# Performance work log

Measured on AMD Instinct MI355X. Metric: run time of the kernel, lower is better.

The kernel has to match this reference:

```python
import jax, jax.numpy as jnp
import numpy as np

EPS = 1e-6


def setup_inputs() -> dict:
    key = jax.random.key(0)
    kH, kE1, kE2, kM, kW = jax.random.split(key, 5)
    B, N, D, E, L = 16, 2048, 64, 32768, 2
    H = jax.random.normal(kH, (B, N, D), dtype=jnp.float32)
    src = jax.random.randint(kE1, (B, 1, E), 0, N)
    dst = jax.random.randint(kE2, (B, 1, E), 0, N)
    edge_index = jnp.concatenate([src, dst], axis=1)  # [B, 2, E]
    m = jax.random.uniform(kM, (B, E), dtype=jnp.float32)
    W = jax.random.normal(kW, (L, D, D), dtype=jnp.float32) * (1.0 / np.sqrt(D))
    return {"H": H, "edge_index": edge_index, "m": m, "W": W}


def reference(H, edge_index, m, W):
    # H: [B, N, D]; edge_index: [B, 2, E] int; m: [B, E]; W: [L, D, D]
    B, N, _ = H.shape
    L = W.shape[0]
    bidx = jnp.arange(B)[:, None]          # [B, 1] broadcasts against [B, E]
    src = edge_index[:, 0, :]
    dst = edge_index[:, 1, :]
    A = jnp.zeros((B, N, N), dtype=H.dtype)
    # batched scatter: A[b, src, dst] = m; A[b, dst, src] = m (symmetric fill)
    A = A.at[bidx, src, dst].set(m)
    A = A.at[bidx, dst, src].set(m)
    A = A + jnp.eye(N, dtype=H.dtype)[None]  # add self loops
    deg = jnp.clip(A.sum(axis=-1), EPS)       # [B, N]
    dis = deg ** -0.5
    A_norm = dis[:, :, None] * A * dis[:, None, :]  # D^-1/2 A D^-1/2
    X = H
    for l in range(L):
        X = jnp.einsum('bnm,bmd->bnd', A_norm, X)
        X = jnp.einsum('bnd,ed->bne', X, W[l])  # Linear: X @ W^T
        if l < L - 1:
            X = jax.nn.gelu(X, approximate=False)  # torch GELU (exact erf); dropout in eval mode
    return X
```

## Files before the change

### kernel.cpp

```cpp
#include <hip/hip_runtime.h>
#include <stdint.h>
#include <math.h>

#define BATCH 16
#define NNODE 2048
#define DDIM  64
#define NEDGE 32768
#define SEG   32
#define SLOTS 128
#define NROWS (BATCH*NNODE)
#define RPB   64

__global__ void k_build(const int* __restrict__ ei, const float* __restrict__ m,
                        uint32_t* __restrict__ cnt4, uint2* __restrict__ entries) {
    __shared__ uint32_t cntS[RPB];
    __shared__ uint32_t keyS[RPB][SEG];
    __shared__ float    valS[RPB][SEG];

    int b  = blockIdx.x & 15;
    int gh = blockIdx.x >> 4;
    int r0 = (gh >> 2) * RPB;
    int q  = gh & 3;
    int t  = threadIdx.x;

    if (t < RPB) cntS[t] = 0u;
    __syncthreads();

    const int*   eb = ei + (size_t)b * 2 * NEDGE;
    const float* mb = m  + (size_t)b * NEDGE;
    int e0 = q * (NEDGE / 4);

    for (int i = 0; i < 8; ++i) {
        int e4 = e0 + i * 1024 + t * 4;
        int4   s4 = *(const int4*)(eb + e4);
        int4   d4 = *(const int4*)(eb + NEDGE + e4);
        float4 m4 = *(const float4*)(mb + e4);
        #pragma unroll
        for (int j = 0; j < 4; ++j) {
            int   src = j == 0 ? s4.x : j == 1 ? s4.y : j == 2 ? s4.z : s4.w;
            int   dst = j == 0 ? d4.x : j == 1 ? d4.y : j == 2 ? d4.z : d4.w;
            float mv  = j == 0 ? m4.x : j == 1 ? m4.y : j == 2 ? m4.z : m4.w;
            int e  = e4 + j;
            int rs = src - r0;
            if ((unsigned)rs < RPB) {
                uint32_t p = atomicAdd(&cntS[rs], 1u);
                if (p < SEG) { keyS[rs][p] = (uint32_t)dst | ((uint32_t)e << 11); valS[rs][p] = mv; }
            }
            int rd = dst - r0;
            if ((unsigned)rd < RPB) {
                uint32_t p = atomicAdd(&cntS[rd], 1u);
                if (p < SEG) { keyS[rd][p] = (uint32_t)src | ((uint32_t)(NEDGE + e) << 11); valS[rd][p] = mv; }
            }
        }
    }
    __syncthreads();

    int lane = t & 63;
    int wid  = t >> 6;
    int pos  = lane & 31;
    int sub  = lane >> 5;
    for (int rr = 0; rr < 8; ++rr) {
        int r  = wid * 16 + rr * 2 + sub;
        int rg = b * NNODE + r0 + r;
        int k  = (int)min(cntS[r], (uint32_t)SEG);
        size_t base = (size_t)rg * SLOTS + q * SEG;
        if (pos < k)
            entries[base + pos] = make_uint2(keyS[r][pos], __float_as_uint(valS[r][pos]));
        if (pos == 0) cnt4[rg * 4 + q] = (uint32_t)k;
    }
}

__global__ void k_dedupe(const uint32_t* __restrict__ cnt4, uint2* __restrict__ entries,
                         uint32_t* __restrict__ cnt_fin,
                         float* __restrict__ dis, float* __restrict__ self) {
    int b    = blockIdx.x & 15;
    int w    = b * NNODE + (blockIdx.x >> 4) * 4 + (threadIdx.x >> 6);
    int lane = threadIdx.x & 63;
    uint4 kq = ((const uint4*)cnt4)[w];
    int k0 = (int)kq.x, k1 = (int)kq.y, k2 = (int)kq.z, k3 = (int)kq.w;
    size_t base = (size_t)w * SLOTS;
    int pos = lane & 31;
    int klo = (lane < 32) ? k0 : k1;
    int khi = (lane < 32) ? k2 : k3;

    uint32_t key0 = 0u, key1 = 0u;
    float v0 = 0.f, v1 = 0.f;
    bool a0 = pos < klo;
    bool a1 = pos < khi;
    if (a0) { uint2 kv = entries[base + lane];      key0 = kv.x; v0 = __uint_as_float(kv.y); }
    if (a1) { uint2 kv = entries[base + 64 + lane]; key1 = kv.x; v1 = __uint_as_float(kv.y); }
    uint32_t c0 = key0 & 2047u, p0 = key0 >> 11;
    uint32_t c1 = key1 & 2047u, p1 = key1 >> 11;

    #define KILL(ks) { uint32_t cs = (ks) & 2047u, ps = (ks) >> 11; \
        a0 = a0 && !((c0 == cs) && (p0 < ps)); \
        a1 = a1 && !((c1 == cs) && (p1 < ps)); }
    for (int s = 0; s < k0; ++s) KILL(__builtin_amdgcn_readlane(key0, s))
    for (int s = 0; s < k1; ++s) KILL(__builtin_amdgcn_readlane(key0, 32 + s))
    for (int s = 0; s < k2; ++s) KILL(__builtin_amdgcn_readlane(key1, s))
    for (int s = 0; s < k3; ++s) KILL(__builtin_amdgcn_readlane(key1, 32 + s))
    #undef KILL

    float sum = (a0 ? v0 : 0.f) + (a1 ? v1 : 0.f);
    for (int off = 32; off; off >>= 1) sum += __shfl_xor(sum, off, 64);
    float deg = fmaxf(1.0f + sum, 1e-6f);
    if (lane == 0) {
        float di = 1.0f / sqrtf(deg);
        dis[w]  = di;
        self[w] = di * di;
    }

    unsigned long long m0 = __ballot(a0);
    unsigned long long m1 = __ballot(a1);
    unsigned long long below = (1ull << lane) - 1ull;
    int n0 = __popcll(m0);
    if (a0) entries[base + __popcll(m0 & below)]      = make_uint2(key0, __float_as_uint(v0));
    if (a1) entries[base + n0 + __popcll(m1 & below)] = make_uint2(key1, __float_as_uint(v1));
    if (lane == 0) cnt_fin[w] = (uint32_t)(n0 + __popcll(m1));
}

__global__ void k_layer(const float* __restrict__ Xin, const float* __restrict__ W,
                        float* __restrict__ Xout,
                        const uint32_t* __restrict__ cnt_fin, const uint2* __restrict__ entries,
                        const float* __restrict__ dis, const float* __restrict__ self,
                        int dogelu) {
    __shared__ float WT[64 * 65];
    int Lb = blockIdx.x;
    int b  = Lb & 15;
    int rb = Lb >> 4;
    int t  = threadIdx.x;

    #pragma unroll
    for (int i = 0; i < 16; ++i) {
        int idx = i * 256 + t;
        WT[(idx & 63) * 65 + (idx >> 6)] = W[idx];
    }
    __syncthreads();

    int lane = t & 63;
    int wid  = t >> 6;
    const float* Xb   = Xin + (size_t)b * NNODE * DDIM;
    const char*  Xc   = (const char*)Xb + lane * 4;
    const float* disB = dis + (b << 11);

    float accv[2];
    #pragma unroll
    for (int rr = 0; rr < 2; ++rr) {
        int row = rb * 8 + wid * 2 + rr;
        int rg  = b * NNODE + row;
        int k   = (int)cnt_fin[rg];
        size_t base = (size_t)rg * SLOTS;

        uint32_t kA = 0u, vA = 0u, kB = 0u, vB = 0u;
        if (lane < k)      { uint2 kv = entries[base + lane];      kA = kv.x; vA = kv.y; }
        if (lane + 64 < k) { uint2 kv = entries[base + 64 + lane]; kB = kv.x; vB = kv.y; }

        float dr = disB[row];
        int   colA = (int)(kA & 2047u);
        uint32_t offA = (uint32_t)colA << 8;
        uint32_t wAu  = __float_as_uint(__uint_as_float(vA) * dr * disB[colA]);
        int   colB = (int)(kB & 2047u);
        uint32_t offB = (uint32_t)colB << 8;
        uint32_t wBu  = __float_as_uint(__uint_as_float(vB) * dr * disB[colB]);

        float acc0 = self[rg] * Xb[(size_t)row * DDIM + lane];
        float acc1 = 0.f, acc2 = 0.f, acc3 = 0.f;

        int k0 = k < 64 ? k : 64;
        int e = 0;
        for (; e + 16 <= k0; e += 16) {
            float xv0, xv1, xv2, xv3, xv4, xv5, xv6, xv7;
            float xv8, xv9, xva, xvb, xvc, xvd, xve, xvf;
            float w0, w1, w2, w3, w4, w5, w6, w7;
            float w8, w9, wa, wb, wc, wd, we, wf;
            #define G(idx, X, Wv) { \
                uint32_t o = __builtin_amdgcn_readlane(offA, e + idx); \
                Wv = __uint_as_float(__builtin_amdgcn_readlane(wAu, e + idx)); \
                X = *(const float*)(Xc + o); }
            G(0, xv0, w0)  G(1, xv1, w1)  G(2, xv2, w2)  G(3, xv3, w3)
            G(4, xv4, w4)  G(5, xv5, w5)  G(6, xv6, w6)  G(7, xv7, w7)
            G(8, xv8, w8)  G(9, xv9, w9)  G(10, xva, wa) G(11, xvb, wb)
            G(12, xvc, wc) G(13, xvd, wd) G(14, xve, we) G(15, xvf, wf)
            #undef G
            acc0 = fmaf(w0, xv0, acc0); acc1 = fmaf(w1, xv1, acc1);
            acc2 = fmaf(w2, xv2, acc2); acc3 = fmaf(w3, xv3, acc3);
            acc0 = fmaf(w4, xv4, acc0); acc1 = fmaf(w5, xv5, acc1);
            acc2 = fmaf(w6, xv6, acc2); acc3 = fmaf(w7, xv7, acc3);
            acc0 = fmaf(w8, xv8, acc0); acc1 = fmaf(w9, xv9, acc1);
            acc2 = fmaf(wa, xva, acc2); acc3 = fmaf(wb, xvb, acc3);
            acc0 = fmaf(wc, xvc, acc0); acc1 = fmaf(wd, xvd, acc1);
            acc2 = fmaf(we, xve, acc2); acc3 = fmaf(wf, xvf, acc3);
        }
        for (; e + 4 <= k0; e += 4) {
            uint32_t o0 = __builtin_amdgcn_readlane(offA, e);
            uint32_t o1 = __builtin_amdgcn_readlane(offA, e + 1);
            uint32_t o2 = __builtin_amdgcn_readlane(offA, e + 2);
            uint32_t o3 = __builtin_amdgcn_readlane(offA, e + 3);
            float w0 = __uint_as_float(__builtin_amdgcn_readlane(wAu, e));
            float w1 = __uint_as_float(__builtin_amdgcn_readlane(wAu, e + 1));
            float w2 = __uint_as_float(__builtin_amdgcn_readlane(wAu, e + 2));
            float w3 = __uint_as_float(__builtin_amdgcn_readlane(wAu, e + 3));
            acc0 = fmaf(w0, *(const float*)(Xc + o0), acc0);
            acc1 = fmaf(w1, *(const float*)(Xc + o1), acc1);
            acc2 = fmaf(w2, *(const float*)(Xc + o2), acc2);
            acc3 = fmaf(w3, *(const float*)(Xc + o3), acc3);
        }
        for (; e < k0; ++e) {
            uint32_t o = __builtin_amdgcn_readlane(offA, e);
            float wv = __uint_as_float(__builtin_amdgcn_readlane(wAu, e));
            acc0 = fmaf(wv, *(const float*)(Xc + o), acc0);
        }
        for (e = 64; e < k; ++e) {
            uint32_t o = __builtin_amdgcn_readlane(offB, e - 64);
            float wv = __uint_as_float(__builtin_amdgcn_readlane(wBu, e - 64));
            acc1 = fmaf(wv, *(const float*)(Xc + o), acc1);
        }
        accv[rr] = (acc0 + acc1) + (acc2 + acc3);
    }

    float sa = accv[0], sb = accv[1];
    float ya = 0.f, yb = 0.f;
    #pragma unroll
    for (int d = 0; d < 64; ++d) {
        float wt = WT[d * 65 + lane];
        ya = fmaf(__uint_as_float(__builtin_amdgcn_readlane(__float_as_uint(sa), d)), wt, ya);
        yb = fmaf(__uint_as_float(__builtin_amdgcn_readlane(__float_as_uint(sb), d)), wt, yb);
    }
    if (dogelu) {
        ya = 0.5f * ya * (1.0f + erff(ya * 0.70710678118654752440f));
        yb = 0.5f * yb * (1.0f + erff(yb * 0.70710678118654752440f));
    }
    int row0 = rb * 8 + wid * 2;
    Xout[((size_t)b * NNODE + row0)     * DDIM + lane] = ya;
    Xout[((size_t)b * NNODE + row0 + 1) * DDIM + lane] = yb;
}

extern "C" void kernel_launch(void* const* d_in, const int* in_sizes, int n_in,
                              void* d_out, int out_size, void* d_ws, size_t ws_size,
                              hipStream_t stream) {
    const float* H  = (const float*)d_in[0];
    const int*   ei = (const int*)d_in[1];
    const float* m  = (const float*)d_in[2];
    const float* W  = (const float*)d_in[3];
    float* out = (float*)d_out;

    char* ws = (char*)d_ws;
    uint32_t* cnt4    = (uint32_t*)ws;
    uint32_t* cnt_fin = (uint32_t*)(ws + (512 << 10));
    float*    dis     = (float*)(ws + (640 << 10));
    float*    self    = (float*)(ws + (768 << 10));
    uint2*    entries = (uint2*)(ws + (896 << 10));
    float*    X2      = (float*)(ws + (896 << 10) + (size_t)NROWS * SLOTS * 8);

    k_build <<<BATCH * (NNODE / RPB) * 4, 256, 0, stream>>>(ei, m, cnt4, entries);
    k_dedupe<<<NROWS / 4, 256, 0, stream>>>(cnt4, entries, cnt_fin, dis, self);
    k_layer <<<4096, 256, 0, stream>>>(H,  W,        X2,  cnt_fin, entries, dis, self, 1);
    k_layer <<<4096, 256, 0, stream>>>(X2, W + 4096, out, cnt_fin, entries, dis, self, 0);
}
```

Baseline: 173.8 us.

## Fuse all phases into one cooperative persistent kernel with grid syncs

Merges the build, dedupe and two layer kernels into a single cooperative kernel of 1024 blocks that separates the phases with grid.sync(), removing three launch gaps. Each block now handles more rows (RPB 128 and 32 rows per block per layer), and SEG drops from 32 to 30 so the shared scratch fits more blocks per CU. If cooperative launch is unavailable it falls back to four separate kernels. The trade-offs are grid-barrier cost, lower parallelism per phase, and a smaller per-quarter slot cap, which drops more entries when a row overflows.

Measured after the change: 279.5 us. 1.61x slower.

```diff
diff --git a/kernel.cpp b/kernel.cpp
--- a/kernel.cpp
+++ b/kernel.cpp
@@ -1,27 +1,31 @@
 #include <hip/hip_runtime.h>
+#include <hip/hip_cooperative_groups.h>
 #include <stdint.h>
 #include <math.h>
+
+namespace cg = cooperative_groups;
 
 #define BATCH 16
 #define NNODE 2048
 #define DDIM  64
 #define NEDGE 32768
-#define SEG   32
-#define SLOTS 128
+#define SEG   30
+#define SLOTS (4*SEG)
 #define NROWS (BATCH*NNODE)
-#define RPB   64
-
-__global__ void k_build(const int* __restrict__ ei, const float* __restrict__ m,
-                        uint32_t* __restrict__ cnt4, uint2* __restrict__ entries) {
-    __shared__ uint32_t cntS[RPB];
-    __shared__ uint32_t keyS[RPB][SEG];
-    __shared__ float    valS[RPB][SEG];
-
-    int b  = blockIdx.x & 15;
-    int gh = blockIdx.x >> 4;
+#define RPB   128
+#define SMEMW (128 + 2*128*SEG)
+
+__device__ __forceinline__ void phase_build(
+        int idx, int t, const int* __restrict__ ei, const float* __restrict__ m,
+        uint32_t* __restrict__ cnt4, uint2* __restrict__ entries, uint32_t* smem) {
+    uint32_t* cntS = smem;
+    uint32_t* keyS = smem + 128;
+    float*    valS = (float*)(smem + 128 + 128 * SEG);
+
+    int b  = idx & 15;
+    int gh = idx >> 4;
     int r0 = (gh >> 2) * RPB;
     int q  = gh & 3;
-    int t  = threadIdx.x;
 
     if (t < RPB) cntS[t] = 0u;
     __syncthreads();
@@ -44,195 +48,236 @@
             int rs = src - r0;
             if ((unsigned)rs < RPB) {
                 uint32_t p = atomicAdd(&cntS[rs], 1u);
-                if (p < SEG) { keyS[rs][p] = (uint32_t)dst | ((uint32_t)e << 11); valS[rs][p] = mv; }
+                if (p < SEG) { keyS[rs * SEG + p] = (uint32_t)dst | ((uint32_t)e << 11); valS[rs * SEG + p] = mv; }
             }
             int rd = dst - r0;
             if ((unsigned)rd < RPB) {
                 uint32_t p = atomicAdd(&cntS[rd], 1u);
-                if (p < SEG) { keyS[rd][p] = (uint32_t)src | ((uint32_t)(NEDGE + e) << 11); valS[rd][p] = mv; }
-            }
-        }
-    }
-    __syncthreads();
-
-    int lane = t & 63;
-    int wid  = t >> 6;
-    int pos  = lane & 31;
-    int sub  = lane >> 5;
-    for (int rr = 0; rr < 8; ++rr) {
-        int r  = wid * 16 + rr * 2 + sub;
+                if (p < SEG) { keyS[rd * SEG + p] = (uint32_t)src | ((uint32_t)(NEDGE + e) << 11); valS[rd * SEG + p] = mv; }
+            }
+        }
+    }
+    __syncthreads();
+
+    int lane = t & 63, wid = t >> 6;
+    int pos = lane & 31, sub = lane >> 5;
+    for (int rr = 0; rr < 16; ++rr) {
+        int r  = wid * 32 + rr * 2 + sub;
         int rg = b * NNODE + r0 + r;
         int k  = (int)min(cntS[r], (uint32_t)SEG);
         size_t base = (size_t)rg * SLOTS + q * SEG;
         if (pos < k)
-            entries[base + pos] = make_uint2(keyS[r][pos], __float_as_uint(valS[r][pos]));
+            entries[base + pos] = make_uint2(keyS[r * SEG + pos], __float_as_uint(valS[r * SEG + pos]));
         if (pos == 0) cnt4[rg * 4 + q] = (uint32_t)k;
     }
 }
 
-__global__ void k_dedupe(const uint32_t* __restrict__ cnt4, uint2* __restrict__ entries,
-                         uint32_t* __restrict__ cnt_fin,
-                         float* __restrict__ dis, float* __restrict__ self) {
-    int b    = blockIdx.x & 15;
-    int w    = b * NNODE + (blockIdx.x >> 4) * 4 + (threadIdx.x >> 6);
-    int lane = threadIdx.x & 63;
-    uint4 kq = ((const uint4*)cnt4)[w];
-    int k0 = (int)kq.x, k1 = (int)kq.y, k2 = (int)kq.z, k3 = (int)kq.w;
-    size_t base = (size_t)w * SLOTS;
-    int pos = lane & 31;
-    int klo = (lane < 32) ? k0 : k1;
-    int khi = (lane < 32) ? k2 : k3;
-
-    uint32_t key0 = 0u, key1 = 0u;
-    float v0 = 0.f, v1 = 0.f;
-    bool a0 = pos < klo;
-    bool a1 = pos < khi;
-    if (a0) { uint2 kv = entries[base + lane];      key0 = kv.x; v0 = __uint_as_float(kv.y); }
-    if (a1) { uint2 kv = entries[base + 64 + lane]; key1 = kv.x; v1 = __uint_as_float(kv.y); }
-    uint32_t c0 = key0 & 2047u, p0 = key0 >> 11;
-    uint32_t c1 = key1 & 2047u, p1 = key1 >> 11;
-
-    #define KILL(ks) { uint32_t cs = (ks) & 2047u, ps = (ks) >> 11; \
-        a0 = a0 && !((c0 == cs) && (p0 < ps)); \
-        a1 = a1 && !((c1 == cs) && (p1 < ps)); }
-    for (int s = 0; s < k0; ++s) KILL(__builtin_amdgcn_readlane(key0, s))
-    for (int s = 0; s < k1; ++s) KILL(__builtin_amdgcn_readlane(key0, 32 + s))
-    for (int s = 0; s < k2; ++s) KILL(__builtin_amdgcn_readlane(key1, s))
-    for (int s = 0; s < k3; ++s) KILL(__builtin_amdgcn_readlane(key1, 32 + s))
-    #undef KILL
-
-    float sum = (a0 ? v0 : 0.f) + (a1 ? v1 : 0.f);
-    for (int off = 32; off; off >>= 1) sum += __shfl_xor(sum, off, 64);
-    float deg = fmaxf(1.0f + sum, 1e-6f);
-    if (lane == 0) {
-        float di = 1.0f / sqrtf(deg);
-        dis[w]  = di;
-        self[w] = di * di;
-    }
-
-    unsigned long long m0 = __ballot(a0);
-    unsigned long long m1 = __ballot(a1);
-    unsigned long long below = (1ull << lane) - 1ull;
-    int n0 = __popcll(m0);
-    if (a0) entries[base + __popcll(m0 & below)]      = make_uint2(key0, __float_as_uint(v0));
-    if (a1) entries[base + n0 + __popcll(m1 & below)] = make_uint2(key1, __float_as_uint(v1));
-    if (lane == 0) cnt_fin[w] = (uint32_t)(n0 + __popcll(m1));
-}
-
-__global__ void k_layer(const float* __restrict__ Xin, const float* __restrict__ W,
-                        float* __restrict__ Xout,
-                        const uint32_t* __restrict__ cnt_fin, const uint2* __restrict__ entries,
-                        const float* __restrict__ dis, const float* __restrict__ self,
-                        int dogelu) {
-    __shared__ float WT[64 * 65];
-    int Lb = blockIdx.x;
-    int b  = Lb & 15;
-    int rb = Lb >> 4;
-    int t  = threadIdx.x;
-
+__device__ __forceinline__ void phase_dedupe(
+        int idx, int t, const uint32_t* __restrict__ cnt4, uint2* __restrict__ entries,
+        uint32_t* __restrict__ cnt_fin, float* __restrict__ dis, float* __restrict__ self) {
+    int b = idx & 15;
+    int lane = t & 63, wid = t >> 6;
+    int pos = lane & 31, sub = lane >> 5;
+    int rowBase = (idx >> 4) * 32 + wid * 8;
+    for (int rr = 0; rr < 8; ++rr) {
+        int w = b * NNODE + rowBase + rr;
+        uint4 kq = ((const uint4*)cnt4)[w];
+        int k0 = (int)kq.x, k1 = (int)kq.y, k2 = (int)kq.z, k3 = (int)kq.w;
+        size_t base = (size_t)w * SLOTS;
+        int klo = sub ? k1 : k0;
+        int khi = sub ? k3 : k2;
+
+        uint32_t key0 = 0u, key1 = 0u;
+        float v0 = 0.f, v1 = 0.f;
+        bool a0 = pos < klo;
+        bool a1 = pos < khi;
+        if (a0) { uint2 kv = entries[base + sub * SEG + pos];           key0 = kv.x; v0 = __uint_as_float(kv.y); }
+        if (a1) { uint2 kv = entries[base + 2 * SEG + sub * SEG + pos]; key1 = kv.x; v1 = __uint_as_float(kv.y); }
+        uint32_t c0 = key0 & 2047u, p0 = key0 >> 11;
+        uint32_t c1 = key1 & 2047u, p1 = key1 >> 11;
+
+        #define KILL(ks) { uint32_t cs = (ks) & 2047u, ps = (ks) >> 11; \
+            a0 = a0 && !((c0 == cs) && (p0 < ps)); \
+            a1 = a1 && !((c1 == cs) && (p1 < ps)); }
+        for (int s = 0; s < k0; ++s) KILL(__builtin_amdgcn_readlane(key0, s))
+        for (int s = 0; s < k1; ++s) KILL(__builtin_amdgcn_readlane(key0, 32 + s))
+        for (int s = 0; s < k2; ++s) KILL(__builtin_amdgcn_readlane(key1, s))
+        for (int s = 0; s < k3; ++s) KILL(__builtin_amdgcn_readlane(key1, 32 + s))
+        #undef KILL
+
+        float sum = (a0 ? v0 : 0.f) + (a1 ? v1 : 0.f);
+        for (int off = 32; off; off >>= 1) sum += __shfl_xor(sum, off, 64);
+        float deg = fmaxf(1.0f + sum, 1e-6f);
+        if (lane == 0) {
+            float di = 1.0f / sqrtf(deg);
+            dis[w]  = di;
+            self[w] = di * di;
+        }
+
+        unsigned long long m0 = __ballot(a0);
+        unsigned long long m1 = __ballot(a1);
+        unsigned long long below = (1ull << lane) - 1ull;
+        int n0 = __popcll(m0);
+        if (a0) entries[base + __popcll(m0 & below)]      = make_uint2(key0, __float_as_uint(v0));
+        if (a1) entries[base + n0 + __popcll(m1 & below)] = make_uint2(key1, __float_as_uint(v1));
+        if (lane == 0) cnt_fin[w] = (uint32_t)(n0 + __popcll(m1));
+    }
+}
+
+__device__ __forceinline__ void phase_layer(
+        int idx, int t, const float* __restrict__ Xin, const float* __restrict__ Wl,
+        float* __restrict__ Xout, const uint32_t* __restrict__ cnt_fin,
+        const uint2* __restrict__ entries, const float* __restrict__ dis,
+        const float* __restrict__ self, int dogelu, float* WT) {
+    int b = idx & 15;
+    int t_ = t;
     #pragma unroll
     for (int i = 0; i < 16; ++i) {
-        int idx = i * 256 + t;
-        WT[(idx & 63) * 65 + (idx >> 6)] = W[idx];
-    }
-    __syncthreads();
-
-    int lane = t & 63;
-    int wid  = t >> 6;
+        int id2 = i * 256 + t_;
+        WT[(id2 & 63) * 65 + (id2 >> 6)] = Wl[id2];
+    }
+    __syncthreads();
+
+    int lane = t & 63, wid = t >> 6;
     const float* Xb   = Xin + (size_t)b * NNODE * DDIM;
     const char*  Xc   = (const char*)Xb + lane * 4;
     const float* disB = dis + (b << 11);
-
-    float accv[2];
-    #pragma unroll
-    for (int rr = 0; rr < 2; ++rr) {
-        int row = rb * 8 + wid * 2 + rr;
-        int rg  = b * NNODE + row;
-        int k   = (int)cnt_fin[rg];
-        size_t base = (size_t)rg * SLOTS;
-
-        uint32_t kA = 0u, vA = 0u, kB = 0u, vB = 0u;
-        if (lane < k)      { uint2 kv = entries[base + lane];      kA = kv.x; vA = kv.y; }
-        if (lane + 64 < k) { uint2 kv = entries[base + 64 + lane]; kB = kv.x; vB = kv.y; }
-
-        float dr = disB[row];
-        int   colA = (int)(kA & 2047u);
-        uint32_t offA = (uint32_t)colA << 8;
-        uint32_t wAu  = __float_as_uint(__uint_as_float(vA) * dr * disB[colA]);
-        int   colB = (int)(kB & 2047u);
-        uint32_t offB = (uint32_t)colB << 8;
-        uint32_t wBu  = __float_as_uint(__uint_as_float(vB) * dr * disB[colB]);
-
-        float acc0 = self[rg] * Xb[(size_t)row * DDIM + lane];
-        float acc1 = 0.f, acc2 = 0.f, acc3 = 0.f;
-
-        int k0 = k < 64 ? k : 64;
-        int e = 0;
-        for (; e + 16 <= k0; e += 16) {
-            float xv0, xv1, xv2, xv3, xv4, xv5, xv6, xv7;
-            float xv8, xv9, xva, xvb, xvc, xvd, xve, xvf;
-            float w0, w1, w2, w3, w4, w5, w6, w7;
-            float w8, w9, wa, wb, wc, wd, we, wf;
-            #define G(idx, X, Wv) { \
-                uint32_t o = __builtin_amdgcn_readlane(offA, e + idx); \
-                Wv = __uint_as_float(__builtin_amdgcn_readlane(wAu, e + idx)); \
-                X = *(const float*)(Xc + o); }
-            G(0, xv0, w0)  G(1, xv1, w1)  G(2, xv2, w2)  G(3, xv3, w3)
-            G(4, xv4, w4)  G(5, xv5, w5)  G(6, xv6, w6)  G(7, xv7, w7)
-            G(8, xv8, w8)  G(9, xv9, w9)  G(10, xva, wa) G(11, xvb, wb)
-            G(12, xvc, wc) G(13, xvd, wd) G(14, xve, we) G(15, xvf, wf)
-            #undef G
-            acc0 = fmaf(w0, xv0, acc0); acc1 = fmaf(w1, xv1, acc1);
-            acc2 = fmaf(w2, xv2, acc2); acc3 = fmaf(w3, xv3, acc3);
-            acc0 = fmaf(w4, xv4, acc0); acc1 = fmaf(w5, xv5, acc1);
-            acc2 = fmaf(w6, xv6, acc2); acc3 = fmaf(w7, xv7, acc3);
-            acc0 = fmaf(w8, xv8, acc0); acc1 = fmaf(w9, xv9, acc1);
-            acc2 = fmaf(wa, xva, acc2); acc3 = fmaf(wb, xvb, acc3);
-            acc0 = fmaf(wc, xvc, acc0); acc1 = fmaf(wd, xvd, acc1);
-            acc2 = fmaf(we, xve, acc2); acc3 = fmaf(wf, xvf, acc3);
-        }
-        for (; e + 4 <= k0; e += 4) {
-            uint32_t o0 = __builtin_amdgcn_readlane(offA, e);
-            uint32_t o1 = __builtin_amdgcn_readlane(offA, e + 1);
-            uint32_t o2 = __builtin_amdgcn_readlane(offA, e + 2);
-            uint32_t o3 = __builtin_amdgcn_readlane(offA, e + 3);
-            float w0 = __uint_as_float(__builtin_amdgcn_readlane(wAu, e));
-            float w1 = __uint_as_float(__builtin_amdgcn_readlane(wAu, e + 1));
-            float w2 = __uint_as_float(__builtin_amdgcn_readlane(wAu, e + 2));
-            float w3 = __uint_as_float(__builtin_amdgcn_readlane(wAu, e + 3));
-            acc0 = fmaf(w0, *(const float*)(Xc + o0), acc0);
-            acc1 = fmaf(w1, *(const float*)(Xc + o1), acc1);
-            acc2 = fmaf(w2, *(const float*)(Xc + o2), acc2);
-            acc3 = fmaf(w3, *(const float*)(Xc + o3), acc3);
-        }
-        for (; e < k0; ++e) {
-            uint32_t o = __builtin_amdgcn_readlane(offA, e);
-            float wv = __uint_as_float(__builtin_amdgcn_readlane(wAu, e));
-            acc0 = fmaf(wv, *(const float*)(Xc + o), acc0);
-        }
-        for (e = 64; e < k; ++e) {
-            uint32_t o = __builtin_amdgcn_readlane(offB, e - 64);
-            float wv = __uint_as_float(__builtin_amdgcn_readlane(wBu, e - 64));
-            acc1 = fmaf(wv, *(const float*)(Xc + o), acc1);
-        }
-        accv[rr] = (acc0 + acc1) + (acc2 + acc3);
-    }
-
-    float sa = accv[0], sb = accv[1];
-    float ya = 0.f, yb = 0.f;
-    #pragma unroll
-    for (int d = 0; d < 64; ++d) {
-        float wt = WT[d * 65 + lane];
-        ya = fmaf(__uint_as_float(__builtin_amdgcn_readlane(__float_as_uint(sa), d)), wt, ya);
-        yb = fmaf(__uint_as_float(__builtin_amdgcn_readlane(__float_as_uint(sb), d)), wt, yb);
-    }
-    if (dogelu) {
-        ya = 0.5f * ya * (1.0f + erff(ya * 0.70710678118654752440f));
-        yb = 0.5f * yb * (1.0f + erff(yb * 0.70710678118654752440f));
-    }
-    int row0 = rb * 8 + wid * 2;
-    Xout[((size_t)b * NNODE + row0)     * DDIM + lane] = ya;
-    Xout[((size_t)b * NNODE + row0 + 1) * DDIM + lane] = yb;
+    int rowBase = (idx >> 4) * 32;
+
+    for (int rp = 0; rp < 4; ++rp) {
+        float accv[2];
+        #pragma unroll
+        for (int rr = 0; rr < 2; ++rr) {
+            int row = rowBase + wid * 8 + rp * 2 + rr;
+            int rg  = b * NNODE + row;
+            int k   = (int)cnt_fin[rg];
+            size_t base = (size_t)rg * SLOTS;
+
+            uint32_t kA = 0u, vA = 0u, kB = 0u, vB = 0u;
+            if (lane < k)      { uint2 kv = entries[base + lane];      kA = kv.x; vA = kv.y; }
+            if (lane + 64 < k) { uint2 kv = entries[base + 64 + lane]; kB = kv.x; vB = kv.y; }
+
+            float dr = disB[row];
+            int   colA = (int)(kA & 2047u);
+            uint32_t offA = (uint32_t)colA << 8;
+            uint32_t wAu  = __float_as_uint(__uint_as_float(vA) * dr * disB[colA]);
+            int   colB = (int)(kB & 2047u);
+            uint32_t offB = (uint32_t)colB << 8;
+            uint32_t wBu  = __float_as_uint(__uint_as_float(vB) * dr * disB[colB]);
+
+            float acc0 = self[rg] * Xb[(size_t)row * DDIM + lane];
+            float acc1 = 0.f, acc2 = 0.f, acc3 = 0.f;
+
+            int k0 = k < 64 ? k : 64;
+            int e = 0;
+            for (; e + 16 <= k0; e += 16) {
+                float xv0, xv1, xv2, xv3, xv4, xv5, xv6, xv7;
+                float xv8, xv9, xva, xvb, xvc, xvd, xve, xvf;
+                float w0, w1, w2, w3, w4, w5, w6, w7;
+                float w8, w9, wa, wb, wc, wd, we, wf;
+                #define G(i2, X, Wv) { \
+                    uint32_t o = __builtin_amdgcn_readlane(offA, e + i2); \
+                    Wv = __uint_as_float(__builtin_amdgcn_readlane(wAu, e + i2)); \
+                    X = *(const float*)(Xc + o); }
+                G(0, xv0, w0)  G(1, xv1, w1)  G(2, xv2, w2)  G(3, xv3, w3)
+                G(4, xv4, w4)  G(5, xv5, w5)  G(6, xv6, w6)  G(7, xv7, w7)
+                G(8, xv8, w8)  G(9, xv9, w9)  G(10, xva, wa) G(11, xvb, wb)
+                G(12, xvc, wc) G(13, xvd, wd) G(14, xve, we) G(15, xvf, wf)
+                #undef G
+                acc0 = fmaf(w0, xv0, acc0); acc1 = fmaf(w1, xv1, acc1);
+                acc2 = fmaf(w2, xv2, acc2); acc3 = fmaf(w3, xv3, acc3);
+                acc0 = fmaf(w4, xv4, acc0); acc1 = fmaf(w5, xv5, acc1);
+                acc2 = fmaf(w6, xv6, acc2); acc3 = fmaf(w7, xv7, acc3);
+                acc0 = fmaf(w8, xv8, acc0); acc1 = fmaf(w9, xv9, acc1);
+                acc2 = fmaf(wa, xva, acc2); acc3 = fmaf(wb, xvb, acc3);
+                acc0 = fmaf(wc, xvc, acc0); acc1 = fmaf(wd, xvd, acc1);
+                acc2 = fmaf(we, xve, acc2); acc3 = fmaf(wf, xvf, acc3);
+            }
+            for (; e + 4 <= k0; e += 4) {
+                uint32_t o0 = __builtin_amdgcn_readlane(offA, e);
+                uint32_t o1 = __builtin_amdgcn_readlane(offA, e + 1);
+                uint32_t o2 = __builtin_amdgcn_readlane(offA, e + 2);
+                uint32_t o3 = __builtin_amdgcn_readlane(offA, e + 3);
+                float w0 = __uint_as_float(__builtin_amdgcn_readlane(wAu, e));
+                float w1 = __uint_as_float(__builtin_amdgcn_readlane(wAu, e + 1));
+                float w2 = __uint_as_float(__builtin_amdgcn_readlane(wAu, e + 2));
+                float w3 = __uint_as_float(__builtin_amdgcn_readlane(wAu, e + 3));
+                acc0 = fmaf(w0, *(const float*)(Xc + o0), acc0);
+                acc1 = fmaf(w1, *(const float*)(Xc + o1), acc1);
+                acc2 = fmaf(w2, *(const float*)(Xc + o2), acc2);
+                acc3 = fmaf(w3, *(const float*)(Xc + o3), acc3);
+            }
+            for (; e < k0; ++e) {
+                uint32_t o = __builtin_amdgcn_readlane(offA, e);
+                float wv = __uint_as_float(__builtin_amdgcn_readlane(wAu, e));
+                acc0 = fmaf(wv, *(const float*)(Xc + o), acc0);
+            }
+            for (e = 64; e < k; ++e) {
+                uint32_t o = __builtin_amdgcn_readlane(offB, e - 64);
+                float wv = __uint_as_float(__builtin_amdgcn_readlane(wBu, e - 64));
+                acc1 = fmaf(wv, *(const float*)(Xc + o), acc1);
+            }
+            accv[rr] = (acc0 + acc1) + (acc2 + acc3);
+        }
+
+        float sa = accv[0], sb = accv[1];
+        float ya = 0.f, yb = 0.f;
+        #pragma unroll
+        for (int d = 0; d < 64; ++d) {
+            float wt = WT[d * 65 + lane];
+            ya = fmaf(__uint_as_float(__builtin_amdgcn_readlane(__float_as_uint(sa), d)), wt, ya);
+            yb = fmaf(__uint_as_float(__builtin_amdgcn_readlane(__float_as_uint(sb), d)), wt, yb);
+        }
+        if (dogelu) {
+            ya = 0.5f * ya * (1.0f + erff(ya * 0.70710678118654752440f));
+            yb = 0.5f * yb * (1.0f + erff(yb * 0.70710678118654752440f));
+        }
+        int row0 = rowBase + wid * 8 + rp * 2;
+        Xout[((size_t)b * NNODE + row0)     * DDIM + lane] = ya;
+        Xout[((size_t)b * NNODE + row0 + 1) * DDIM + lane] = yb;
+    }
+}
+
+__global__ void __launch_bounds__(256, 5)
+k_all(const int* __restrict__ ei, const float* __restrict__ m,
+      const float* __restrict__ H, const float* __restrict__ W,
+      float* __restrict__ X2, float* __restrict__ out,
+      uint32_t* __restrict__ cnt4, uint32_t* __restrict__ cnt_fin,
+      float* __restrict__ dis, float* __restrict__ self,
+      uint2* __restrict__ entries) {
+    __shared__ uint32_t smem[SMEMW];
+    cg::grid_group grid = cg::this_grid();
+    int idx = blockIdx.x, t = threadIdx.x;
+
+    phase_build(idx, t, ei, m, cnt4, entries, smem);
+    grid.sync();
+    phase_dedupe(idx, t, cnt4, entries, cnt_fin, dis, self);
+    grid.sync();
+    __syncthreads();
+    phase_layer(idx, t, H, W, X2, cnt_fin, entries, dis, self, 1, (float*)smem);
+    grid.sync();
+    __syncthreads();
+    phase_layer(idx, t, X2, W + 4096, out, cnt_fin, entries, dis, self, 0, (float*)smem);
+}
+
+__global__ void __launch_bounds__(256, 4)
+k_build_s(const int* __restrict__ ei, const float* __restrict__ m,
+          uint32_t* __restrict__ cnt4, uint2* __restrict__ entries) {
+    __shared__ uint32_t smem[SMEMW];
+    phase_build(blockIdx.x, threadIdx.x, ei, m, cnt4, entries, smem);
+}
+__global__ void __launch_bounds__(256, 4)
+k_dedupe_s(const uint32_t* __restrict__ cnt4, uint2* __restrict__ entries,
+           uint32_t* __restrict__ cnt_fin, float* __restrict__ dis, float* __restrict__ self) {
+    phase_dedupe(blockIdx.x, threadIdx.x, cnt4, entries, cnt_fin, dis, self);
+}
+__global__ void __launch_bounds__(256, 4)
+k_layer_s(const float* __restrict__ Xin, const float* __restrict__ W,
+          float* __restrict__ Xout, const uint32_t* __restrict__ cnt_fin,
+          const uint2* __restrict__ entries, const float* __restrict__ dis,
+          const float* __restrict__ self, int dogelu) {
+    __shared__ float WT[64 * 65];
+    phase_layer(blockIdx.x, threadIdx.x, Xin, W, Xout, cnt_fin, entries, dis, self, dogelu, WT);
 }
 
 extern "C" void kernel_launch(void* const* d_in, const int* in_sizes, int n_in,
@@ -252,8 +297,24 @@
     uint2*    entries = (uint2*)(ws + (896 << 10));
     float*    X2      = (float*)(ws + (896 << 10) + (size_t)NROWS * SLOTS * 8);
 
-    k_build <<<BATCH * (NNODE / RPB) * 4, 256, 0, stream>>>(ei, m, cnt4, entries);
-    k_dedupe<<<NROWS / 4, 256, 0, stream>>>(cnt4, entries, cnt_fin, dis, self);
-    k_layer <<<4096, 256, 0, stream>>>(H,  W,        X2,  cnt_fin, entries, dis, self, 1);
-    k_layer <<<4096, 256, 0, stream>>>(X2, W + 4096, out, cnt_fin, entries, dis, self, 0);
-}
+    int dev = 0;
+    hipGetDevice(&dev);
+    int coop = 0;
+    hipDeviceGetAttribute(&coop, hipDeviceAttributeCooperativeLaunch, dev);
+    int maxb = 0;
+    hipOccupancyMaxActiveBlocksPerMultiprocessor(&maxb, k_all, 256, 0);
+
+    if (coop && maxb >= 4) {
+        void* args[] = {
+            (void*)&ei, (void*)&m, (void*)&H, (void*)&W, (void*)&X2, (void*)&out,
+            (void*)&cnt4, (void*)&cnt_fin, (void*)&dis, (void*)&self, (void*)&entries
+        };
+        hipError_t err = hipLaunchCooperativeKernel((const void*)k_all, dim3(1024), dim3(256),
+                                                    args, 0, stream);
+        if (err == hipSuccess) return;
+    }
+    k_build_s <<<1024, 256, 0, stream>>>(ei, m, cnt4, entries);
+    k_dedupe_s<<<1024, 256, 0, stream>>>(cnt4, entries, cnt_fin, dis, self);
+    k_layer_s <<<1024, 256, 0, stream>>>(H,  W,        X2,  cnt_fin, entries, dis, self, 1);
+    k_layer_s <<<1024, 256, 0, stream>>>(X2, W + 4096, out, cnt_fin, entries, dis, self, 0);
+}
```
